# Kernel optimization log

Measured on AMD Instinct MI355X. Metric: run time of the kernel, lower is better.

The kernel has to match this reference:

```python
import jax, jax.numpy as jnp
import numpy as np

V = 100000
E = 800000
D = 128
K = 8
EDGE_FEAT = 16
VEH_FEAT_DIM = 8
N_VEH = 16
N_LAYERS = 2
LN_EPS = 1e-5


def _ln(x, g, b):
    m = jnp.mean(x, axis=-1, keepdims=True)
    v = jnp.mean(jnp.square(x - m), axis=-1, keepdims=True)
    return (x - m) * jax.lax.rsqrt(v + LN_EPS) * g + b


def setup_inputs() -> dict:
    key = jax.random.key(0)
    ks = jax.random.split(key, 12)
    s = lambda fan_in: 1.0 / np.sqrt(fan_in)
    return {
        "Z_node_full": jax.random.normal(ks[0], (V, D), jnp.float32),
        "visit_meta": jax.random.uniform(ks[1], (V, 1 + K + 1), jnp.float32),
        "veh_feat": jax.random.normal(ks[2], (N_VEH, VEH_FEAT_DIM), jnp.float32),
        "edge_attr": jax.random.normal(ks[3], (E, EDGE_FEAT), jnp.float32),
        "edge_src": jax.random.randint(ks[4], (E,), 0, V, jnp.int32),
        "edge_dst": jax.random.randint(ks[5], (E,), 0, V, jnp.int32),
        "current_nodes": jax.random.randint(ks[6], (N_VEH,), 0, V, jnp.int32),
        "node_proj_w": jax.random.normal(ks[7], (D + 1 + K + 1, D), jnp.float32) * s(D + 1 + K + 1),
        "node_proj_b": jnp.zeros((D,), jnp.float32),
        "layers_w1": jax.random.normal(ks[8], (N_LAYERS, D + EDGE_FEAT, D), jnp.float32) * s(D + EDGE_FEAT),
        "layers_b1": jnp.zeros((N_LAYERS, D), jnp.float32),
        "layers_w2": jax.random.normal(ks[9], (N_LAYERS, D, D), jnp.float32) * s(D),
        "layers_b2": jnp.zeros((N_LAYERS, D), jnp.float32),
        "layers_ln_g": jnp.ones((N_LAYERS, D), jnp.float32),
        "layers_ln_b": jnp.zeros((N_LAYERS, D), jnp.float32),
        "props_w1": jax.random.normal(ks[10], (VEH_FEAT_DIM, D), jnp.float32) * s(VEH_FEAT_DIM),
        "props_b1": jnp.zeros((D,), jnp.float32),
        "props_w2": jax.random.normal(ks[11], (D, D), jnp.float32) * s(D),
        "props_b2": jnp.zeros((D,), jnp.float32),
        "ro_g": jnp.ones((D,), jnp.float32),
        "ro_b": jnp.zeros((D,), jnp.float32),
    }


def reference(Z_node_full, visit_meta, veh_feat, edge_attr, edge_src, edge_dst,
              current_nodes, node_proj_w, node_proj_b, layers_w1, layers_b1,
              layers_w2, layers_b2, layers_ln_g, layers_ln_b, props_w1, props_b1,
              props_w2, props_b2, ro_g, ro_b):
    # node projection: [V, D+K+2] @ [D+K+2, D]
    h_in = jnp.concatenate([Z_node_full, visit_meta], axis=-1)
    h = h_in @ node_proj_w + node_proj_b

    # per-receiver edge count, clamped to 1 (shared across layers)
    count = jax.ops.segment_sum(jnp.ones((edge_dst.shape[0],), h.dtype), edge_dst,
                                num_segments=h.shape[0])
    count = jnp.maximum(count, 1.0)[:, None]  # [V, 1]

    for l in range(N_LAYERS):
        h_src = h[edge_src]                                   # [E, D] gather
        x = jnp.concatenate([h_src, edge_attr], axis=-1)      # [E, D+edge_feat]
        msg = jax.nn.relu(x @ layers_w1[l] + layers_b1[l]) @ layers_w2[l] + layers_b2[l]
        agg = jax.ops.segment_sum(msg, edge_dst, num_segments=h.shape[0]) / count
        h = _ln(h + agg, layers_ln_g[l], layers_ln_b[l])

    props = jax.nn.relu(veh_feat @ props_w1 + props_b1) @ props_w2 + props_b2
    Z_veh = h[current_nodes]                                  # [N_veh, D] readout gather
    return _ln(Z_veh + props, ro_g, ro_b)
```

## Files before the change

kernel.cpp:

```cpp
#include <hip/hip_runtime.h>
#include <hip/hip_bf16.h>

#define V_N 100000
#define VP  100096
#define E_N 800000
#define NVEH 16
#define LN_EPS 1e-5f
#define NTILES (VP / 64)

typedef unsigned int uint;
typedef unsigned short ushort;
typedef unsigned char uchar;
typedef __attribute__((ext_vector_type(8))) short bf8_t;
typedef __attribute__((ext_vector_type(4))) float f4_t;

__device__ __forceinline__ float bf2f(ushort u) {
    union { uint i; float f; } c; c.i = ((uint)u) << 16; return c.f;
}
__device__ __forceinline__ ushort f2bf(float f) {
    union { float f; uint i; } c; c.f = f; uint x = c.i;
    return (ushort)((x + 0x7FFFu + ((x >> 16) & 1u)) >> 16);
}
__device__ __forceinline__ uint pk2(float a, float b) {
    return (uint)f2bf(a) | ((uint)f2bf(b) << 16);
}

__global__ __launch_bounds__(256) void k_pack(const float* __restrict__ W, uint4* __restrict__ dst,
                                              int nslots, int krows) {
    int slot = blockIdx.x * 256 + threadIdx.x;
    if (slot >= nslots) return;
    int ks = slot >> 9;
    int ct = (slot >> 6) & 7;
    int l  = slot & 63;
    int k0 = ks * 32 + ((l >> 4) << 3);
    int col = (ct << 4) + (l & 15);
    ushort u[8];
#pragma unroll
    for (int e = 0; e < 8; ++e) {
        int k = k0 + e;
        u[e] = (k < krows) ? f2bf(W[(size_t)k * 128 + col]) : (ushort)0;
    }
    uint4 p;
    p.x = (uint)u[0] | ((uint)u[1] << 16);
    p.y = (uint)u[2] | ((uint)u[3] << 16);
    p.z = (uint)u[4] | ((uint)u[5] << 16);
    p.w = (uint)u[6] | ((uint)u[7] << 16);
    dst[slot] = p;
}

__global__ __launch_bounds__(256) void k_count(const int* __restrict__ dst, int* __restrict__ cnt) {
    int i = blockIdx.x * blockDim.x + threadIdx.x;
    if (i < E_N) atomicAdd(&cnt[dst[i]], 1);
}

__global__ __launch_bounds__(256) void k_scan1(const int* __restrict__ cnt, int* __restrict__ rowptr,
                                               int* __restrict__ part) {
    __shared__ int sh[256];
    const int tid = threadIdx.x;
    const int base = blockIdx.x * 1024 + tid * 4;
    int v0 = (base + 0 < V_N) ? cnt[base + 0] : 0;
    int v1 = (base + 1 < V_N) ? cnt[base + 1] : 0;
    int v2 = (base + 2 < V_N) ? cnt[base + 2] : 0;
    int v3 = (base + 3 < V_N) ? cnt[base + 3] : 0;
    int s = v0 + v1 + v2 + v3;
    sh[tid] = s; __syncthreads();
    for (int off = 1; off < 256; off <<= 1) {
        int t = (tid >= off) ? sh[tid - off] : 0;
        __syncthreads();
        sh[tid] += t;
        __syncthreads();
    }
    int excl = sh[tid] - s;
    if (tid == 255) part[blockIdx.x] = sh[255];
    int run = excl;
    if (base + 0 < V_N) rowptr[base + 0] = run; run += v0;
    if (base + 1 < V_N) rowptr[base + 1] = run; run += v1;
    if (base + 2 < V_N) rowptr[base + 2] = run; run += v2;
    if (base + 3 < V_N) rowptr[base + 3] = run;
}

__global__ __launch_bounds__(128) void k_scan2(const int* __restrict__ part, int* __restrict__ pex, int nb) {
    __shared__ int sh[128];
    const int tid = threadIdx.x;
    int v = (tid < nb) ? part[tid] : 0;
    sh[tid] = v; __syncthreads();
    for (int off = 1; off < 128; off <<= 1) {
        int t = (tid >= off) ? sh[tid - off] : 0;
        __syncthreads();
        sh[tid] += t;
        __syncthreads();
    }
    if (tid < nb) pex[tid] = sh[tid] - v;
}

__global__ __launch_bounds__(256) void k_scan3(int* __restrict__ rowptr, const int* __restrict__ pex,
                                               int* __restrict__ cursor) {
    int i = blockIdx.x * 256 + threadIdx.x;
    if (i < V_N) {
        int rp = rowptr[i] + pex[i >> 10];
        rowptr[i] = rp;
        cursor[i] = rp;
    }
    if (i == 0) rowptr[V_N] = E_N;
}

__global__ __launch_bounds__(256) void k_scatter(const int* __restrict__ src, const int* __restrict__ dst,
                                                 int* __restrict__ cursor, int2* __restrict__ pes) {
    int e = blockIdx.x * 256 + threadIdx.x;
    if (e < E_N) {
        int d = dst[e];
        int p = atomicAdd(&cursor[d], 1);
        pes[p] = make_int2(e, src[e]);
    }
}

__global__ __launch_bounds__(256) void k_nodeproj(const float* __restrict__ Z, const float* __restrict__ meta,
                                                  const uint4* __restrict__ Bpk, const float* __restrict__ b,
                                                  ushort* __restrict__ hb) {
    __shared__ uint4 Bs4[2560];
    const int tid = threadIdx.x;
    for (int slot = tid; slot < 2560; slot += 256) Bs4[slot] = Bpk[slot];
    __syncthreads();
    const int lane = tid & 63, wid = tid >> 6;
    const int l15 = lane & 15, l4 = lane >> 4;
    float bcol[8];
#pragma unroll
    for (int ct = 0; ct < 8; ++ct) bcol[ct] = b[ct * 16 + l15];
    const int tile = blockIdx.x;
    int rowA = tile * 64 + wid * 16 + l15;
    int rowAc = rowA < V_N ? rowA : V_N - 1;
    const float* zp = Z + (size_t)rowAc * 128;
    union { uint4 u; bf8_t b; } afr[5];
#pragma unroll
    for (int ks = 0; ks < 4; ++ks) {
        int k0 = ks * 32 + l4 * 8;
        float4 f0 = *(const float4*)(zp + k0);
        float4 f1 = *(const float4*)(zp + k0 + 4);
        afr[ks].u.x = pk2(f0.x, f0.y);
        afr[ks].u.y = pk2(f0.z, f0.w);
        afr[ks].u.z = pk2(f1.x, f1.y);
        afr[ks].u.w = pk2(f1.z, f1.w);
    }
    {
        const float* mp = meta + (size_t)rowAc * 10;
        int f0 = l4 * 8;
        ushort u[8];
#pragma unroll
        for (int e = 0; e < 8; ++e) {
            int f = f0 + e;
            u[e] = (f < 10) ? f2bf(mp[f]) : (ushort)0;
        }
        afr[4].u.x = (uint)u[0] | ((uint)u[1] << 16);
        afr[4].u.y = (uint)u[2] | ((uint)u[3] << 16);
        afr[4].u.z = (uint)u[4] | ((uint)u[5] << 16);
        afr[4].u.w = (uint)u[6] | ((uint)u[7] << 16);
    }
    f4_t acc[8];
#pragma unroll
    for (int ct = 0; ct < 8; ++ct) acc[ct] = (f4_t){bcol[ct], bcol[ct], bcol[ct], bcol[ct]};
#pragma unroll
    for (int ks = 0; ks < 5; ++ks) {
#pragma unroll
        for (int ct = 0; ct < 8; ++ct) {
            union { uint4 u; bf8_t b; } cb; cb.u = Bs4[(ks * 8 + ct) * 64 + lane];
            acc[ct] = __builtin_amdgcn_mfma_f32_16x16x32_bf16(afr[ks].b, cb.b, acc[ct], 0, 0, 0);
        }
    }
    const int rowC0 = tile * 64 + wid * 16 + l4 * 4;
#pragma unroll
    for (int ct = 0; ct < 8; ++ct) {
        int col = ct * 16 + l15;
#pragma unroll
        for (int r = 0; r < 4; ++r) {
            int row = rowC0 + r;
            if (row < V_N) hb[(size_t)row * 128 + col] = f2bf(acc[ct][r]);
        }
    }
}

__global__ __launch_bounds__(256) void k_gemm1(const ushort* __restrict__ hb, const uint4* __restrict__ Bpk,
                                               const float* __restrict__ b, ushort* __restrict__ tb) {
    __shared__ uint4 Bs4[2048];
    const int tid = threadIdx.x;
    for (int slot = tid; slot < 2048; slot += 256) Bs4[slot] = Bpk[slot];
    __syncthreads();
    const int lane = tid & 63, wid = tid >> 6;
    const int l15 = lane & 15, l4 = lane >> 4;
    float bcol[8];
#pragma unroll
    for (int ct = 0; ct < 8; ++ct) bcol[ct] = b[ct * 16 + l15];
    const int tile = blockIdx.x;
    const int rowA = tile * 64 + wid * 16 + l15;
    const uint4* ap = (const uint4*)(hb + (size_t)rowA * 128);
    f4_t acc[8];
#pragma unroll
    for (int ct = 0; ct < 8; ++ct) acc[ct] = (f4_t){bcol[ct], bcol[ct], bcol[ct], bcol[ct]};
#pragma unroll
    for (int ks = 0; ks < 4; ++ks) {
        union { uint4 u; bf8_t b; } ca; ca.u = ap[ks * 4 + l4];
#pragma unroll
        for (int ct = 0; ct < 8; ++ct) {
            union { uint4 u; bf8_t b; } cb; cb.u = Bs4[(ks * 8 + ct) * 64 + lane];
            acc[ct] = __builtin_amdgcn_mfma_f32_16x16x32_bf16(ca.b, cb.b, acc[ct], 0, 0, 0);
        }
    }
    const int rowC0 = tile * 64 + wid * 16 + l4 * 4;
#pragma unroll
    for (int ct = 0; ct < 8; ++ct) {
        int col = ct * 16 + l15;
#pragma unroll
        for (int r = 0; r < 4; ++r) {
            int row = rowC0 + r;
            if (row < V_N) tb[(size_t)row * 128 + col] = f2bf(acc[ct][r]);
        }
    }
}

__global__ __launch_bounds__(256) void k_edge_mlp(const float* __restrict__ ea,
                                                  const int2* __restrict__ pes,
                                                  const uint4* __restrict__ Bpk,
                                                  uchar* __restrict__ U) {
    __shared__ uint4 Bs4[512];
    const int tid = threadIdx.x;
    for (int slot = tid; slot < 512; slot += 256) Bs4[slot] = Bpk[slot];
    __syncthreads();
    const int lane = tid & 63, wid = tid >> 6;
    const int l15 = lane & 15, l4 = lane >> 4;
    const long ebase = (long)blockIdx.x * 64 + wid * 16;
    union { uint4 u; bf8_t b; } afr;
    afr.u = make_uint4(0u, 0u, 0u, 0u);
    if (l4 < 2) {
        int eidx = pes[ebase + l15].x;
        const float* ep = ea + (size_t)eidx * 16 + l4 * 8;
        float4 f0 = *(const float4*)ep;
        float4 f1 = *(const float4*)(ep + 4);
        afr.u.x = pk2(f0.x, f0.y);
        afr.u.y = pk2(f0.z, f0.w);
        afr.u.z = pk2(f1.x, f1.y);
        afr.u.w = pk2(f1.z, f1.w);
    }
    f4_t acc[8];
#pragma unroll
    for (int ct = 0; ct < 8; ++ct) acc[ct] = (f4_t){0.f, 0.f, 0.f, 0.f};
#pragma unroll
    for (int ct = 0; ct < 8; ++ct) {
        union { uint4 u; bf8_t b; } cb; cb.u = Bs4[ct * 64 + lane];
        acc[ct] = __builtin_amdgcn_mfma_f32_16x16x32_bf16(afr.b, cb.b, acc[ct], 0, 0, 0);
    }
    const long rowC0 = ebase + l4 * 4;
#pragma unroll
    for (int r = 0; r < 4; ++r) {
        int p01 = __builtin_amdgcn_cvt_pk_fp8_f32(acc[0][r], acc[1][r], 0, false);
        int p23 = __builtin_amdgcn_cvt_pk_fp8_f32(acc[2][r], acc[3][r], 0, false);
        int p45 = __builtin_amdgcn_cvt_pk_fp8_f32(acc[4][r], acc[5][r], 0, false);
        int p67 = __builtin_amdgcn_cvt_pk_fp8_f32(acc[6][r], acc[7][r], 0, false);
        uint2 w;
        w.x = ((uint)p01 & 0xffffu) | ((uint)p23 << 16);
        w.y = ((uint)p45 & 0xffffu) | ((uint)p67 << 16);
        *(uint2*)(U + (size_t)(rowC0 + r) * 128 + l15 * 8) = w;
    }
}

__global__ __launch_bounds__(256) void k_edge_agg2(const ushort* __restrict__ tb,
                                                   const uchar* __restrict__ U,
                                                   const int2* __restrict__ pes,
                                                   const int* __restrict__ rowptr,
                                                   ushort* __restrict__ S) {
    const int lane = threadIdx.x & 63;
    const int wid  = threadIdx.x >> 6;
    const int v = blockIdx.x * 4 + wid;
    if (v >= V_N) return;
    const int st = rowptr[v], en = rowptr[v + 1];
    const int co = 2 * lane;
    const int s0 = (co & 15) * 8 + (co >> 4);
    float a0 = 0.f, a1 = 0.f;
    for (int i0 = st; i0 < en; i0 += 8) {
        const int n = en - i0;
        int idx[8];
#pragma unroll
        for (int j = 0; j < 8; ++j) idx[j] = (j < n) ? (i0 + j) : i0;
        int s[8];
#pragma unroll
        for (int j = 0; j < 8; ++j) s[j] = pes[idx[j]].y;
        uint tv[8]; uint uv[8];
#pragma unroll
        for (int j = 0; j < 8; ++j) {
            tv[j] = *(const uint*)(tb + (size_t)s[j] * 128 + co);
            const uchar* up = U + (size_t)idx[j] * 128 + s0;
            uv[j] = (uint)up[0] | ((uint)up[8] << 8);
        }
#pragma unroll
        for (int j = 0; j < 8; ++j) {
            auto uf = __builtin_amdgcn_cvt_pk_f32_fp8((int)uv[j], false);
            float p0 = bf2f((ushort)(tv[j] & 0xffffu)) + uf[0];
            float p1 = bf2f((ushort)(tv[j] >> 16)) + uf[1];
            if (j < n) { a0 += fmaxf(p0, 0.f); a1 += fmaxf(p1, 0.f); }
        }
    }
    int dg = en - st;
    float inv = 1.f / (float)(dg > 1 ? dg : 1);
    *(uint*)(S + (size_t)v * 128 + co) = pk2(a0 * inv, a1 * inv);
}

__global__ __launch_bounds__(256) void k_node_update(const ushort* __restrict__ S, ushort* __restrict__ hb,
                                                     const int* __restrict__ cnt,
                                                     const uint4* __restrict__ Bpk, const float* __restrict__ b2,
                                                     const float* __restrict__ g, const float* __restrict__ bt) {
    __shared__ uint4 Bs4[2048];
    const int tid = threadIdx.x;
    for (int slot = tid; slot < 2048; slot += 256) Bs4[slot] = Bpk[slot];
    __syncthreads();
    const int lane = tid & 63, wid = tid >> 6;
    const int l15 = lane & 15, l4 = lane >> 4;
    float b2c[8], gc[8], btc[8];
#pragma unroll
    for (int ct = 0; ct < 8; ++ct) {
        int col = ct * 16 + l15;
        b2c[ct] = b2[col]; gc[ct] = g[col]; btc[ct] = bt[col];
    }
    const int tile = blockIdx.x;
    const int rowA = tile * 64 + wid * 16 + l15;
    const uint4* ap = (const uint4*)(S + (size_t)rowA * 128);
    f4_t acc[8];
#pragma unroll
    for (int ct = 0; ct < 8; ++ct) acc[ct] = (f4_t){0.f, 0.f, 0.f, 0.f};
#pragma unroll
    for (int ks = 0; ks < 4; ++ks) {
        union { uint4 u; bf8_t b; } ca; ca.u = ap[ks * 4 + l4];
#pragma unroll
        for (int ct = 0; ct < 8; ++ct) {
            union { uint4 u; bf8_t b; } cb; cb.u = Bs4[(ks * 8 + ct) * 64 + lane];
            acc[ct] = __builtin_amdgcn_mfma_f32_16x16x32_bf16(ca.b, cb.b, acc[ct], 0, 0, 0);
        }
    }
    const int rowC0 = tile * 64 + wid * 16 + l4 * 4;
    float mask[4];
#pragma unroll
    for (int r = 0; r < 4; ++r) {
        int row = rowC0 + r;
        int dg = (row < V_N) ? cnt[row] : 0;
        mask[r] = (dg > 0) ? 1.f : 0.f;
    }
    float x[8][4];
#pragma unroll
    for (int ct = 0; ct < 8; ++ct) {
        int col = ct * 16 + l15;
#pragma unroll
        for (int r = 0; r < 4; ++r) {
            float hv = bf2f(hb[(size_t)(rowC0 + r) * 128 + col]);
            x[ct][r] = hv + acc[ct][r] + b2c[ct] * mask[r];
        }
    }
#pragma unroll
    for (int r = 0; r < 4; ++r) {
        float s = 0.f;
#pragma unroll
        for (int ct = 0; ct < 8; ++ct) s += x[ct][r];
        s += __shfl_xor(s, 1); s += __shfl_xor(s, 2);
        s += __shfl_xor(s, 4); s += __shfl_xor(s, 8);
        float mean = s * (1.f / 128.f);
        float vv = 0.f;
#pragma unroll
        for (int ct = 0; ct < 8; ++ct) { float d = x[ct][r] - mean; vv = fmaf(d, d, vv); }
        vv += __shfl_xor(vv, 1); vv += __shfl_xor(vv, 2);
        vv += __shfl_xor(vv, 4); vv += __shfl_xor(vv, 8);
        float rs = rsqrtf(vv * (1.f / 128.f) + LN_EPS);
        int row = rowC0 + r;
        bool ok = row < V_N;
#pragma unroll
        for (int ct = 0; ct < 8; ++ct) {
            int col = ct * 16 + l15;
            float y = (x[ct][r] - mean) * rs * gc[ct] + btc[ct];
            if (ok) hb[(size_t)row * 128 + col] = f2bf(y);
        }
    }
}

__global__ __launch_bounds__(128) void k_final(const ushort* __restrict__ hb, const int* __restrict__ cur,
                                               const float* __restrict__ veh,
                                               const float* __restrict__ pw1, const float* __restrict__ pb1,
                                               const float* __restrict__ pw2, const float* __restrict__ pb2,
                                               const float* __restrict__ g, const float* __restrict__ bt,
                                               float* __restrict__ out) {
    __shared__ float hid[128];
    __shared__ float red[2];
    const int i = blockIdx.x;
    const int j = threadIdx.x;
    float a = pb1[j];
#pragma unroll
    for (int f = 0; f < 8; ++f) a = fmaf(veh[i * 8 + f], pw1[f * 128 + j], a);
    hid[j] = fmaxf(a, 0.f);
    __syncthreads();
    float o = pb2[j] + bf2f(hb[(size_t)cur[i] * 128 + j]);
    for (int k = 0; k < 128; ++k) o = fmaf(hid[k], pw2[k * 128 + j], o);
    const int lane = j & 63, wid = j >> 6;
    float s = o;
#pragma unroll
    for (int off = 32; off > 0; off >>= 1) s += __shfl_xor(s, off);
    if (lane == 0) red[wid] = s;
    __syncthreads();
    float mean = (red[0] + red[1]) * (1.f / 128.f);
    __syncthreads();
    float d = o - mean;
    float vv = d * d;
#pragma unroll
    for (int off = 32; off > 0; off >>= 1) vv += __shfl_xor(vv, off);
    if (lane == 0) red[wid] = vv;
    __syncthreads();
    float var = (red[0] + red[1]) * (1.f / 128.f);
    float r = rsqrtf(var + LN_EPS);
    out[i * 128 + j] = d * r * g[j] + bt[j];
}

extern "C" void kernel_launch(void* const* d_in, const int* in_sizes, int n_in,
                              void* d_out, int out_size, void* d_ws, size_t ws_size,
                              hipStream_t stream) {
    const float* Z    = (const float*)d_in[0];
    const float* meta = (const float*)d_in[1];
    const float* veh  = (const float*)d_in[2];
    const float* ea   = (const float*)d_in[3];
    const int*   esrc = (const int*)d_in[4];
    const int*   edst = (const int*)d_in[5];
    const int*   cur  = (const int*)d_in[6];
    const float* npw  = (const float*)d_in[7];
    const float* npb  = (const float*)d_in[8];
    const float* w1   = (const float*)d_in[9];
    const float* b1   = (const float*)d_in[10];
    const float* w2   = (const float*)d_in[11];
    const float* b2   = (const float*)d_in[12];
    const float* lng  = (const float*)d_in[13];
    const float* lnb  = (const float*)d_in[14];
    const float* pw1  = (const float*)d_in[15];
    const float* pb1  = (const float*)d_in[16];
    const float* pw2  = (const float*)d_in[17];
    const float* pb2  = (const float*)d_in[18];
    const float* rog  = (const float*)d_in[19];
    const float* rob  = (const float*)d_in[20];

    ushort* hb = (ushort*)d_ws;
    ushort* tb = hb + (size_t)VP * 128;
    ushort* S  = tb + (size_t)VP * 128;
    int* cnt    = (int*)(S + (size_t)VP * 128);
    int* rowptr = cnt + VP;
    int* cursor = rowptr + VP;
    int2* pes   = (int2*)(cursor + VP);
    int* part   = (int*)(pes + E_N);
    int* pex    = part + 128;
    uint4* Bnp  = (uint4*)(pex + 128);
    uint4* Bw1b = Bnp + 2560;
    uint4* Bw1a = Bw1b + 2 * 2048;
    uint4* Bw2  = Bw1a + 2 * 512;
    uchar* U    = (uchar*)(Bw2 + 2 * 2048);
    float* out = (float*)d_out;

    const int NB = (V_N + 1023) / 1024;

    k_pack<<<10, 256, 0, stream>>>(npw, Bnp, 2560, 138);
    for (int l = 0; l < 2; ++l) {
        const float* W1b = w1 + (size_t)l * 144 * 128;
        const float* W1a = W1b + 128 * 128;
        k_pack<<<8, 256, 0, stream>>>(W1b, Bw1b + l * 2048, 2048, 128);
        k_pack<<<2, 256, 0, stream>>>(W1a, Bw1a + l * 512, 512, 16);
        k_pack<<<8, 256, 0, stream>>>(w2 + (size_t)l * 128 * 128, Bw2 + l * 2048, 2048, 128);
    }

    hipMemsetAsync(cnt, 0, VP * sizeof(int), stream);
    k_count<<<(E_N + 255) / 256, 256, 0, stream>>>(edst, cnt);
    k_scan1<<<NB, 256, 0, stream>>>(cnt, rowptr, part);
    k_scan2<<<1, 128, 0, stream>>>(part, pex, NB);
    k_scan3<<<(V_N + 255) / 256, 256, 0, stream>>>(rowptr, pex, cursor);
    k_scatter<<<(E_N + 255) / 256, 256, 0, stream>>>(esrc, edst, cursor, pes);
    k_nodeproj<<<NTILES, 256, 0, stream>>>(Z, meta, Bnp, npb, hb);

    for (int l = 0; l < 2; ++l) {
        k_gemm1<<<NTILES, 256, 0, stream>>>(hb, Bw1b + l * 2048, b1 + l * 128, tb);
        k_edge_mlp<<<E_N / 64, 256, 0, stream>>>(ea, pes, Bw1a + l * 512, U);
        k_edge_agg2<<<V_N / 4, 256, 0, stream>>>(tb, U, pes, rowptr, S);
        k_node_update<<<NTILES, 256, 0, stream>>>(S, hb, cnt, Bw2 + l * 2048,
                                                  b2 + l * 128, lng + l * 128, lnb + l * 128);
    }
    k_final<<<NVEH, 128, 0, stream>>>(hb, cur, veh, pw1, pb1, pw2, pb2, rog, rob, out);
}
```

Measured before the change: 607.8 us.

## Store node tables in MFMA-native permuted layout for vectorized writes and reads

The node transform kernel now writes each row's eight column-tile values as one 16-byte store in a permuted column layout, instead of scattered 2-byte stores. The edge aggregation kernel reads that permuted layout directly, so each lane loads adjacent fp8 bytes with one 16-bit load instead of two strided byte loads. Its output S is written back in the permuted-to-logical order using two scalar stores. This trades a coalesced S write for fewer and wider gather loads on the hot edge path, and it depends on the U and tb permutations matching exactly.

```diff
diff --git a/kernel.cpp b/kernel.cpp
--- a/kernel.cpp
+++ b/kernel.cpp
@@ -206,12 +206,15 @@
     }
     const int rowC0 = tile * 64 + wid * 16 + l4 * 4;
 #pragma unroll
-    for (int ct = 0; ct < 8; ++ct) {
-        int col = ct * 16 + l15;
-#pragma unroll
-        for (int r = 0; r < 4; ++r) {
-            int row = rowC0 + r;
-            if (row < V_N) tb[(size_t)row * 128 + col] = f2bf(acc[ct][r]);
+    for (int r = 0; r < 4; ++r) {
+        int row = rowC0 + r;
+        if (row < V_N) {
+            uint4 w;
+            w.x = pk2(acc[0][r], acc[1][r]);
+            w.y = pk2(acc[2][r], acc[3][r]);
+            w.z = pk2(acc[4][r], acc[5][r]);
+            w.w = pk2(acc[6][r], acc[7][r]);
+            *(uint4*)(tb + (size_t)row * 128 + l15 * 8) = w;
         }
     }
 }
@@ -271,8 +274,8 @@
     const int v = blockIdx.x * 4 + wid;
     if (v >= V_N) return;
     const int st = rowptr[v], en = rowptr[v + 1];
-    const int co = 2 * lane;
-    const int s0 = (co & 15) * 8 + (co >> 4);
+    const int p0 = 2 * lane;
+    const int c0 = ((p0 & 7) << 4) | (p0 >> 3);
     float a0 = 0.f, a1 = 0.f;
     for (int i0 = st; i0 < en; i0 += 8) {
         const int n = en - i0;
@@ -282,24 +285,24 @@
         int s[8];
 #pragma unroll
         for (int j = 0; j < 8; ++j) s[j] = pes[idx[j]].y;
-        uint tv[8]; uint uv[8];
+        uint tv[8]; ushort uv[8];
 #pragma unroll
         for (int j = 0; j < 8; ++j) {
-            tv[j] = *(const uint*)(tb + (size_t)s[j] * 128 + co);
-            const uchar* up = U + (size_t)idx[j] * 128 + s0;
-            uv[j] = (uint)up[0] | ((uint)up[8] << 8);
+            tv[j] = *(const uint*)(tb + (size_t)s[j] * 128 + p0);
+            uv[j] = *(const ushort*)(U + (size_t)idx[j] * 128 + p0);
         }
 #pragma unroll
         for (int j = 0; j < 8; ++j) {
             auto uf = __builtin_amdgcn_cvt_pk_f32_fp8((int)uv[j], false);
-            float p0 = bf2f((ushort)(tv[j] & 0xffffu)) + uf[0];
-            float p1 = bf2f((ushort)(tv[j] >> 16)) + uf[1];
-            if (j < n) { a0 += fmaxf(p0, 0.f); a1 += fmaxf(p1, 0.f); }
+            float q0 = bf2f((ushort)(tv[j] & 0xffffu)) + uf[0];
+            float q1 = bf2f((ushort)(tv[j] >> 16)) + uf[1];
+            if (j < n) { a0 += fmaxf(q0, 0.f); a1 += fmaxf(q1, 0.f); }
         }
     }
     int dg = en - st;
     float inv = 1.f / (float)(dg > 1 ? dg : 1);
-    *(uint*)(S + (size_t)v * 128 + co) = pk2(a0 * inv, a1 * inv);
+    S[(size_t)v * 128 + c0]      = f2bf(a0 * inv);
+    S[(size_t)v * 128 + c0 + 16] = f2bf(a1 * inv);
 }
 
 __global__ __launch_bounds__(256) void k_node_update(const ushort* __restrict__ S, ushort* __restrict__ hb,
```

Result: faster. 543.2 us (-10.6%).
